# Kernel optimization log

Measured on AMD Instinct MI355X. Metric: run time of the kernel, lower is better.

The kernel has to match this reference:

```python
import jax, jax.numpy as jnp
import numpy as np

B, S, D, H, F, L, V, SPAN = 4, 1024, 1024, 16, 4096, 4, 32000, 512
DH = D // H
NEG = -1e9


def _ln(x, g, b, eps=1e-12):
    m = x.mean(-1, keepdims=True)
    v = ((x - m) ** 2).mean(-1, keepdims=True)
    return (x - m) * jax.lax.rsqrt(v + eps) * g + b


def setup_inputs() -> dict:
    key = jax.random.key(0)
    ks = iter(jax.random.split(key, 40))
    g = lambda shape: jax.random.normal(next(ks), shape, jnp.float32) * 0.02
    inp = {
        "input_ids": jax.random.randint(next(ks), (B, S), 0, V),
        "segment_ids": jnp.zeros((B, S), jnp.int32),
        "attention_mask": jnp.ones((B, S), jnp.float32),
        "tok_emb": g((V, D)),
        "seg_emb": g((2, D)),
        "emb_ln_g": jnp.ones((D,), jnp.float32),
        "emb_ln_b": jnp.zeros((D,), jnp.float32),
        "rel_emb": g((2 * SPAN, D)),
        "Wq": g((L, D, D)), "bq": jnp.zeros((L, D), jnp.float32),
        "Wk": g((L, D, D)), "bk": jnp.zeros((L, D), jnp.float32),
        "Wv": g((L, D, D)), "bv": jnp.zeros((L, D), jnp.float32),
        "Wo": g((L, D, D)), "bo": jnp.zeros((L, D), jnp.float32),
        "ln1_g": jnp.ones((L, D), jnp.float32), "ln1_b": jnp.zeros((L, D), jnp.float32),
        "W1": g((L, D, F)), "b1": jnp.zeros((L, F), jnp.float32),
        "W2": g((L, F, D)), "b2": jnp.zeros((L, D), jnp.float32),
        "ln2_g": jnp.ones((L, D), jnp.float32), "ln2_b": jnp.zeros((L, D), jnp.float32),
    }
    return inp


def _forward(input_ids, segment_ids, attention_mask, tok_emb, seg_emb, emb_ln_g,
             emb_ln_b, rel_emb, Wq, bq, Wk, bk, Wv, bv, Wo, bo, ln1_g, ln1_b,
             W1, b1, W2, b2, ln2_g, ln2_b):
    # BertEmbedding (max_len=0 => no absolute positions): token + segment, LN, mask
    h = _ln(tok_emb[input_ids] + seg_emb[segment_ids], emb_ln_g, emb_ln_b)
    h = h * attention_mask[..., None]

    # relative positions (bucket_size=0 path): rel[q,k] = q - k, clamped into table
    pos = jnp.arange(S)
    rel = pos[:, None] - pos[None, :]                      # [S,S]
    c2p_idx = jnp.clip(rel + SPAN, 0, 2 * SPAN - 1)        # [S,S]
    p2c_idx = jnp.clip(-rel + SPAN, 0, 2 * SPAN - 1)       # [S,S]
    bias = (1.0 - attention_mask)[:, None, None, :] * NEG  # [B,1,1,S] additive mask

    scale = 1.0 / jnp.sqrt(jnp.asarray(DH * 3, h.dtype))   # scale_factor = 1 + |{c2p,p2c}|

    def layer(h, p):
        wq, bq_, wk, bk_, wv, bv_, wo, bo_, g1, b1n, w1, b1f, w2, b2f, g2, b2n = p
        q = (h @ wq + bq_).reshape(B, S, H, DH)
        k = (h @ wk + bk_).reshape(B, S, H, DH)
        v = (h @ wv + bv_).reshape(B, S, H, DH)
        att = jnp.einsum('bqhd,bkhd->bhqk', q, k) * scale
        # disentangled relative-position bias (shared q/k projections on rel table)
        pos_k = (rel_emb @ wk + bk_).reshape(2 * SPAN, H, DH)
        pos_q = (rel_emb @ wq + bq_).reshape(2 * SPAN, H, DH)
        c2p = jnp.einsum('bqhd,phd->bhqp', q, pos_k) * scale   # [B,H,S,2*SPAN]
        att = att + jnp.take_along_axis(c2p, c2p_idx[None, None], axis=-1)
        p2c = jnp.einsum('bkhd,phd->bhkp', k, pos_q) * scale   # [B,H,S,2*SPAN]
        att = att + jnp.swapaxes(
            jnp.take_along_axis(p2c, p2c_idx[None, None], axis=-1), -1, -2)
        probs = jax.nn.softmax(att + bias, axis=-1)
        ctx = jnp.einsum('bhqk,bkhd->bqhd', probs, v).reshape(B, S, D)
        h = _ln(h + ctx @ wo + bo_, g1, b1n)
        ff = jax.nn.gelu(h @ w1 + b1f, approximate=False) @ w2 + b2f
        return _ln(h + ff, g2, b2n), None

    h, _ = jax.lax.scan(layer, h, (Wq, bq, Wk, bk, Wv, bv, Wo, bo,
                                   ln1_g, ln1_b, W1, b1, W2, b2, ln2_g, ln2_b))
    return h


def reference(input_ids, segment_ids, attention_mask, tok_emb, seg_emb, emb_ln_g,
              emb_ln_b, rel_emb, Wq, bq, Wk, bk, Wv, bv, Wo, bo, ln1_g, ln1_b,
              W1, b1, W2, b2, ln2_g, ln2_b):
    return _forward(input_ids, segment_ids, attention_mask, tok_emb, seg_emb,
                    emb_ln_g, emb_ln_b, rel_emb, Wq, bq, Wk, bk, Wv, bv, Wo, bo,
                    ln1_g, ln1_b, W1, b1, W2, b2, ln2_g, ln2_b)
```

## Files before the change

kernel.cpp:

```cpp
#include <hip/hip_runtime.h>

#define DEV __device__ __forceinline__

typedef __bf16 bf16;
typedef __bf16 bf16x4 __attribute__((ext_vector_type(4)));
typedef __bf16 bf16x8 __attribute__((ext_vector_type(8)));
typedef float f32x4 __attribute__((ext_vector_type(4)));

constexpr int B_ = 4, S_ = 1024, D_ = 1024, H_ = 16, F_ = 4096, L_ = 4, SPAN_ = 512, DH_ = 64;
constexpr float SCALE_ = 0.07216878364870322f;
constexpr float LOG2E_ = 1.4426950408889634f;
constexpr float SCL2_ = SCALE_ * LOG2E_;
constexpr float THR2_ = 11.5f;
constexpr long POSL_ = 32L * 1024 * 64;

DEV void gload_lds16(const void* g, void* l) {
  __builtin_amdgcn_global_load_lds((const __attribute__((address_space(1))) void*)g,
                                   (__attribute__((address_space(3))) void*)l, 16, 0, 0);
}

template <int CTRL>
DEV float dppf(float x) {
  return __builtin_bit_cast(
      float, __builtin_amdgcn_mov_dpp(__builtin_bit_cast(int, x), CTRL, 0xf, 0xf, true));
}
DEV float rowMax16(float v) {
  v = fmaxf(v, dppf<0x128>(v));
  v = fmaxf(v, dppf<0x124>(v));
  v = fmaxf(v, dppf<0x122>(v));
  v = fmaxf(v, dppf<0x121>(v));
  return v;
}
DEV float rowSum16(float v) {
  v += dppf<0x128>(v);
  v += dppf<0x124>(v);
  v += dppf<0x122>(v);
  v += dppf<0x121>(v);
  return v;
}

DEV float blockSum4(float v, volatile float* red) {
#pragma unroll
  for (int o = 32; o; o >>= 1) v += __shfl_xor(v, o);
  if ((threadIdx.x & 63) == 0) red[threadIdx.x >> 6] = v;
  __syncthreads();
  return red[0] + red[1] + red[2] + red[3];
}

DEV bf16x8 lds_frag(const bf16* buf, int row, int chunk) {
  return *(const bf16x8*)((const char*)buf + row * 128 + ((chunk ^ (row & 7)) << 4));
}
DEV bf16x8 rdfrag(const char* base, int row, int chunk) {
  return *(const bf16x8*)(base + row * 128 + ((chunk ^ (row & 7)) << 4));
}

template <int EPI>
__global__ __launch_bounds__(512, 1) void gemm256(
    const bf16* __restrict__ A, const bf16* __restrict__ Bm,
    const float* __restrict__ bias, void* __restrict__ Cout,
    int K, int lda, int ldb, int ldc, long sA, long sB, long sC) {
  extern __shared__ __align__(16) char smem[];

  const int z = blockIdx.z;
  A += (long)z * sA;
  Bm += (long)z * sB;
  const long coff = (long)z * sC;

  const int nwg = gridDim.x * gridDim.y;
  const int flat = blockIdx.y * gridDim.x + blockIdx.x;
  const int qq = nwg >> 3;
  const int swz = (flat & 7) * qq + (flat >> 3);
  const int bx = swz % gridDim.x, by = swz / gridDim.x;
  const int m0 = by * 256, n0 = bx * 256;

  const int tid = threadIdx.x, lane = tid & 63, wave = tid >> 6;
  const int wr = wave >> 2, wc = wave & 3;
  const int fr = lane & 15, fq = lane >> 4;

  f32x4 acc[8][4];
#pragma unroll
  for (int m = 0; m < 8; m++)
#pragma unroll
    for (int n = 0; n < 4; n++) acc[m][n] = f32x4{0.f, 0.f, 0.f, 0.f};

  const int r8 = tid >> 3;
  const int swzel = ((tid & 7) ^ (r8 & 7)) << 3;
  const bf16* ga = A + (long)(m0 + r8) * lda + swzel;
  const bf16* gb = Bm + (long)(n0 + r8) * ldb + swzel;

  const int NT = K >> 6;

  auto stage = [&](int t) {
    const long ko = (long)t * 64;
    char* da = smem + ((t & 1) << 15) + wave * 1024;
    gload_lds16(ga + ko, da);
    gload_lds16(ga + 64 * (long)lda + ko, da + 8192);
    gload_lds16(ga + 128 * (long)lda + ko, da + 16384);
    gload_lds16(ga + 192 * (long)lda + ko, da + 24576);
    char* db = smem + 65536 + ((t & 1) << 15) + wave * 1024;
    gload_lds16(gb + ko, db);
    gload_lds16(gb + 64 * (long)ldb + ko, db + 8192);
    gload_lds16(gb + 128 * (long)ldb + ko, db + 16384);
    gload_lds16(gb + 192 * (long)ldb + ko, db + 24576);
  };

  stage(0);
  asm volatile("s_waitcnt vmcnt(0)" ::: "memory");
  __builtin_amdgcn_s_barrier();

  for (int j = 0; j < NT; j++) {
    const char* Ac = smem + ((j & 1) << 15);
    const char* Bc = smem + 65536 + ((j & 1) << 15);

    if (j + 1 < NT) stage(j + 1);

    bf16x8 af[4][2], bfg[4][2];
#pragma unroll
    for (int m = 0; m < 4; m++) {
      const int ar = wr * 128 + m * 16 + fr;
      af[m][0] = rdfrag(Ac, ar, fq);
      af[m][1] = rdfrag(Ac, ar, 4 + fq);
    }
#pragma unroll
    for (int n = 0; n < 4; n++) {
      const int br = wc * 64 + n * 16 + fr;
      bfg[n][0] = rdfrag(Bc, br, fq);
      bfg[n][1] = rdfrag(Bc, br, 4 + fq);
    }

    __builtin_amdgcn_s_setprio(1);
#pragma unroll
    for (int m = 0; m < 4; m++)
#pragma unroll
      for (int n = 0; n < 4; n++)
#pragma unroll
        for (int kc = 0; kc < 2; kc++)
          acc[m][n] = __builtin_amdgcn_mfma_f32_16x16x32_bf16(af[m][kc], bfg[n][kc],
                                                              acc[m][n], 0, 0, 0);
    __builtin_amdgcn_s_setprio(0);
    __builtin_amdgcn_sched_barrier(0);

#pragma unroll
    for (int m = 0; m < 4; m++) {
      const int ar = wr * 128 + (m + 4) * 16 + fr;
      af[m][0] = rdfrag(Ac, ar, fq);
      af[m][1] = rdfrag(Ac, ar, 4 + fq);
    }
    __builtin_amdgcn_s_setprio(1);
#pragma unroll
    for (int m = 0; m < 4; m++)
#pragma unroll
      for (int n = 0; n < 4; n++)
#pragma unroll
        for (int kc = 0; kc < 2; kc++)
          acc[m + 4][n] = __builtin_amdgcn_mfma_f32_16x16x32_bf16(af[m][kc], bfg[n][kc],
                                                                  acc[m + 4][n], 0, 0, 0);
    __builtin_amdgcn_s_setprio(0);

    asm volatile("s_waitcnt vmcnt(0)" ::: "memory");
    __builtin_amdgcn_s_barrier();
  }

#pragma unroll
  for (int m = 0; m < 8; m++) {
#pragma unroll
    for (int n = 0; n < 4; n++) {
      const int col = n0 + wc * 64 + n * 16 + fr;
      float bval = 0.f;
      if constexpr (EPI == 3 || EPI == 4) bval = bias ? bias[col] : 0.f;
#pragma unroll
      for (int rr = 0; rr < 4; rr++) {
        const int row = m0 + wr * 128 + m * 16 + fq * 4 + rr;
        const long idx = coff + (long)row * ldc + col;
        const float v = acc[m][n][rr];
        if constexpr (EPI == 0) ((float*)Cout)[idx] = v;
        else if constexpr (EPI == 3) ((bf16*)Cout)[idx] = (bf16)(v + bval);
        else if constexpr (EPI == 4) {
          float x = v + bval;
          x = 0.5f * x * (1.f + erff(x * 0.70710678118654752f));
          ((bf16*)Cout)[idx] = (bf16)x;
        }
      }
    }
  }
}

template <int EPI>
__global__ __launch_bounds__(256) void gemm_bt(
    const bf16* __restrict__ A, const bf16* __restrict__ Bm,
    const float* __restrict__ bias, void* __restrict__ Cout,
    int M, int N, int K, int lda, int ldb, int ldc, float alpha,
    long sA, long sB, long sC, long sBias) {
  __shared__ alignas(16) bf16 As[128 * 64];
  __shared__ alignas(16) bf16 Bs[128 * 64];

  const int z = blockIdx.z;
  A += (long)z * sA;
  Bm += (long)z * sB;
  bias += (long)z * sBias;
  const long coff = (long)z * sC;

  const int nwg = gridDim.x * gridDim.y;
  const int flat = blockIdx.y * gridDim.x + blockIdx.x;
  const int qq = nwg >> 3;
  const int swz = (flat & 7) * qq + (flat >> 3);
  const int bx = swz % gridDim.x, by = swz / gridDim.x;

  const int m0 = by * 128, n0 = bx * 128;
  const int tid = threadIdx.x, lane = tid & 63, wave = tid >> 6;
  const int wr = wave >> 1, wc = wave & 1;
  const int fr = lane & 15, fq = lane >> 4;

  f32x4 acc[4][4];
#pragma unroll
  for (int m = 0; m < 4; m++)
#pragma unroll
    for (int n = 0; n < 4; n++) acc[m][n] = f32x4{0.f, 0.f, 0.f, 0.f};

  const int r8 = tid >> 3;
  const int swzel = ((tid & 7) ^ (r8 & 7)) << 3;
  const bf16* ga = A + (long)(m0 + r8) * lda + swzel;
  const bf16* gb = Bm + (long)(n0 + r8) * ldb + swzel;
  const int swzrd = fr & 7;

  for (int k0 = 0; k0 < K; k0 += 64) {
#pragma unroll
    for (int i = 0; i < 4; i++)
      gload_lds16(ga + (long)i * 32 * lda + k0, (char*)As + i * 4096 + wave * 1024);
#pragma unroll
    for (int i = 0; i < 4; i++)
      gload_lds16(gb + (long)i * 32 * ldb + k0, (char*)Bs + i * 4096 + wave * 1024);
    __syncthreads();
#pragma unroll
    for (int kc = 0; kc < 2; kc++) {
      bf16x8 af[4], bfv[4];
#pragma unroll
      for (int m = 0; m < 4; m++)
        af[m] = *(const bf16x8*)((char*)As + (wr * 64 + m * 16 + fr) * 128 +
                                 (((kc * 4 + fq) ^ swzrd) << 4));
#pragma unroll
      for (int n = 0; n < 4; n++)
        bfv[n] = *(const bf16x8*)((char*)Bs + (wc * 64 + n * 16 + fr) * 128 +
                                  (((kc * 4 + fq) ^ swzrd) << 4));
#pragma unroll
      for (int m = 0; m < 4; m++)
#pragma unroll
        for (int n = 0; n < 4; n++)
          acc[m][n] = __builtin_amdgcn_mfma_f32_16x16x32_bf16(af[m], bfv[n], acc[m][n], 0, 0, 0);
    }
    __syncthreads();
  }

#pragma unroll
  for (int m = 0; m < 4; m++) {
#pragma unroll
    for (int n = 0; n < 4; n++) {
      const int col = n0 + wc * 64 + n * 16 + fr;
      float bval = 0.f;
      if constexpr (EPI == 3 || EPI == 4 || EPI == 5) bval = bias ? bias[col] : 0.f;
#pragma unroll
      for (int rr = 0; rr < 4; rr++) {
        const int row = m0 + wr * 64 + m * 16 + fq * 4 + rr;
        const long idx = coff + (long)row * ldc + col;
        const float v = acc[m][n][rr];
        if constexpr (EPI == 0) ((float*)Cout)[idx] = v * alpha;
        else if constexpr (EPI == 3) ((bf16*)Cout)[idx] = (bf16)(v + bval);
        else if constexpr (EPI == 4) {
          float x = v + bval;
          x = 0.5f * x * (1.f + erff(x * 0.70710678118654752f));
          ((bf16*)Cout)[idx] = (bf16)x;
        } else if constexpr (EPI == 5) {
          const long pidx = coff + ((long)(col >> 6) * 1024 + row) * 64 + (col & 63);
          ((bf16*)Cout)[pidx] = (bf16)(v + bval);
        }
      }
    }
  }
}

__global__ __launch_bounds__(256) void repack_kv(const bf16* __restrict__ qkv,
                                                 bf16* __restrict__ kp,
                                                 bf16* __restrict__ vp) {
  const int kt = blockIdx.x, bh = blockIdx.y;
  const int b = bh >> 4, h = bh & 15;
  const int k0 = kt * 64;
  __shared__ bf16 t[64][72];
  const int ty = threadIdx.x >> 3, tx = threadIdx.x & 7;
#pragma unroll
  for (int p = 0; p < 2; p++) {
    const int s = k0 + p * 32 + ty;
    const long base = (long)(b * 1024 + s) * 3072 + h * 64;
    bf16x8 kv = *(const bf16x8*)(qkv + base + 1024 + tx * 8);
    *(bf16x8*)(kp + ((long)(bh * 1024 + s) << 6) + tx * 8) = kv;
    bf16x8 vv = *(const bf16x8*)(qkv + base + 2048 + tx * 8);
    *(bf16x8*)(&t[p * 32 + ty][tx * 8]) = vv;
  }
  __syncthreads();
  const int dh = threadIdx.x >> 2, sc = (threadIdx.x & 3) * 16;
  bf16 tmp[16];
#pragma unroll
  for (int j = 0; j < 16; j++) tmp[j] = t[sc + j][dh];
  bf16* dst = vp + ((long)(bh * 16 + kt) << 12) + dh * 64 + sc;
  *(bf16x8*)dst = *(bf16x8*)tmp;
  *(bf16x8*)(dst + 8) = *(bf16x8*)(tmp + 8);
}

__global__ __launch_bounds__(256) void attn_fused(
    const bf16* __restrict__ qkv, const bf16* __restrict__ kp,
    const bf16* __restrict__ vp, const bf16* __restrict__ pospk,
    const float* __restrict__ mask, bf16* __restrict__ ctx) {
  const int id = blockIdx.x;
  const int xcd = id & 7, sub = id >> 3;
  const int bh = xcd + 8 * (sub >> 4);
  const int qt = sub & 15;
  const int b = bh >> 4, h = bh & 15;
  const int q0 = qt * 64;
  const int tid = threadIdx.x, wave = tid >> 6, lane = tid & 63;
  const int fr = lane & 15, fq = lane >> 4;

  __shared__ alignas(16) char smem[79360];
  bf16* PXk = (bf16*)smem;
  char* p_l = smem;
  bf16* PXq = (bf16*)(smem + 16384);
  bf16* Ks = (bf16*)(smem + 32768);
  bf16* Vs = (bf16*)(smem + 40960);
  bf16* c2p_T = (bf16*)(smem + 49152);
  bf16* p2c_T = (bf16*)(smem + 61952);

  const bf16* posq = pospk + ((long)h << 16);
  const bf16* posk = pospk + ((long)(16 + h) << 16);
  const bf16* kbase = kp + ((long)bh << 16);
  const bf16* vbase = vp + ((long)bh << 16);

  bf16x8 qa[2];
  {
    const bf16* qrow = qkv + (long)(b * 1024 + q0 + wave * 16 + fr) * 3072 + h * 64;
    qa[0] = *(const bf16x8*)(qrow + fq * 8);
    qa[1] = *(const bf16x8*)(qrow + 32 + fq * 8);
  }

  f32x4 o[4];
#pragma unroll
  for (int n = 0; n < 4; n++) o[n] = f32x4{0.f, 0.f, 0.f, 0.f};
  float m_r[4], l_r[4];
#pragma unroll
  for (int r = 0; r < 4; r++) { m_r[r] = -1e30f; l_r[r] = 0.f; }

  char* pl_base = p_l + wave * 2048;
  bf16* c2p_w = c2p_T + wave * 1600;
  const int wbyte = wave * 1024;

  for (int kt = 0; kt < 16; kt++) {
    const int k0 = kt * 64;

    __syncthreads();
    {
      const int j0k = q0 - k0 + 449;
      const int j0q = k0 - q0 + 449;
#pragma unroll
      for (int c = 0; c < 4; c++) {
        const int u = c * 256 + tid;
        const int rr = u >> 3;
        const int sel = (((u & 7) ^ (rr & 7)) << 3);
        int jk = j0k + rr;
        jk = jk < 0 ? 0 : (jk > 1023 ? 1023 : jk);
        gload_lds16(posk + ((long)jk << 6) + sel, (char*)PXk + c * 4096 + wbyte);
        int jq = j0q + rr;
        jq = jq < 0 ? 0 : (jq > 1023 ? 1023 : jq);
        gload_lds16(posq + ((long)jq << 6) + sel, (char*)PXq + c * 4096 + wbyte);
      }
#pragma unroll
      for (int c = 0; c < 2; c++) {
        const int u = c * 256 + tid;
        const int rr = u >> 3;
        const int sel = (((u & 7) ^ (rr & 7)) << 3);
        gload_lds16(kbase + ((long)(k0 + rr) << 6) + sel, (char*)Ks + c * 4096 + wbyte);
        gload_lds16(vbase + ((long)kt << 12) + ((long)rr << 6) + sel,
                    (char*)Vs + c * 4096 + wbyte);
      }
    }
    __syncthreads();

    bf16x8 ka[2];
    ka[0] = lds_frag(Ks, wave * 16 + fr, fq);
    ka[1] = lds_frag(Ks, wave * 16 + fr, 4 + fq);
    __builtin_amdgcn_s_setprio(1);
    {
      f32x4 cw[5];
#pragma unroll
      for (int t = 0; t < 5; t++) cw[t] = f32x4{0.f, 0.f, 0.f, 0.f};
#pragma unroll
      for (int kc = 0; kc < 2; kc++)
#pragma unroll
        for (int t = 0; t < 5; t++) {
          const bf16x8 pb = lds_frag(PXk, wave * 16 + t * 16 + fr, kc * 4 + fq);
          cw[t] = __builtin_amdgcn_mfma_f32_16x16x32_bf16(qa[kc], pb, cw[t], 0, 0, 0);
        }
#pragma unroll
      for (int t = 0; t < 5; t++) {
        bf16x4 pk;
#pragma unroll
        for (int r = 0; r < 4; r++) pk[r] = (bf16)cw[t][r];
        *(bf16x4*)&c2p_w[(t * 16 + fr) * 20 + fq * 4] = pk;
      }
    }
    f32x4 s[4];
#pragma unroll
    for (int n = 0; n < 4; n++) s[n] = f32x4{0.f, 0.f, 0.f, 0.f};
#pragma unroll
    for (int kc = 0; kc < 2; kc++)
#pragma unroll
      for (int n = 0; n < 4; n++) {
        const bf16x8 kb = lds_frag(Ks, n * 16 + fr, kc * 4 + fq);
        s[n] = __builtin_amdgcn_mfma_f32_16x16x32_bf16(qa[kc], kb, s[n], 0, 0, 0);
      }
    {
      f32x4 pw[5];
#pragma unroll
      for (int t = 0; t < 5; t++) pw[t] = f32x4{0.f, 0.f, 0.f, 0.f};
#pragma unroll
      for (int kc = 0; kc < 2; kc++)
#pragma unroll
        for (int t = 0; t < 5; t++) {
          const bf16x8 pb = lds_frag(PXq, (wave + t) * 16 + fr, kc * 4 + fq);
          pw[t] = __builtin_amdgcn_mfma_f32_16x16x32_bf16(ka[kc], pb, pw[t], 0, 0, 0);
        }
#pragma unroll
      for (int t = 0; t < 5; t++) {
        bf16x4 pk;
#pragma unroll
        for (int r = 0; r < 4; r++) pk[r] = (bf16)pw[t][r];
        *(bf16x4*)&p2c_T[((wave + t) * 16 + fr) * 68 + wave * 16 + fq * 4] = pk;
      }
    }
    __builtin_amdgcn_s_setprio(0);
    __syncthreads();

    bf16x8 vb[2][4];
#pragma unroll
    for (int kc = 0; kc < 2; kc++)
#pragma unroll
      for (int n = 0; n < 4; n++) vb[kc][n] = lds_frag(Vs, n * 16 + fr, kc * 4 + fq);

    float st[4][4];
#pragma unroll
    for (int n = 0; n < 4; n++) {
      const int ki = n * 16 + fr;
      const float mb = (1.0f - mask[b * S_ + k0 + ki]) * (-1e9f * LOG2E_);
#pragma unroll
      for (int r = 0; r < 4; r++) {
        const int qi_s = fq * 4 + r;
        const float cv = (float)c2p_w[(qi_s - ki + 63) * 20 + qi_s];
        const float pv = (float)p2c_T[(ki - (wave * 16 + qi_s) + 63) * 68 + ki];
        st[n][r] = (s[n][r] + cv + pv) * SCL2_ + mb;
      }
    }

    float pmax[4];
#pragma unroll
    for (int r = 0; r < 4; r++) {
      float v = fmaxf(fmaxf(st[0][r], st[1][r]), fmaxf(st[2][r], st[3][r]));
      pmax[r] = rowMax16(v);
    }
    const bool ok = (pmax[0] - m_r[0] <= THR2_) && (pmax[1] - m_r[1] <= THR2_) &&
                    (pmax[2] - m_r[2] <= THR2_) && (pmax[3] - m_r[3] <= THR2_);
    if (!__all(ok)) {
#pragma unroll
      for (int r = 0; r < 4; r++) {
        const float mn = fmaxf(m_r[r], pmax[r]);
        const float sc = exp2f(m_r[r] - mn);
        m_r[r] = mn;
        l_r[r] *= sc;
#pragma unroll
        for (int n = 0; n < 4; n++) o[n][r] *= sc;
      }
    }
    float rs[4] = {0.f, 0.f, 0.f, 0.f};
#pragma unroll
    for (int n = 0; n < 4; n++) {
      const int ki = n * 16 + fr;
#pragma unroll
      for (int r = 0; r < 4; r++) {
        const int qi_s = fq * 4 + r;
        const float p = exp2f(st[n][r] - m_r[r]);
        rs[r] += p;
        *(bf16*)(pl_base + qi_s * 128 + ((ki * 2) ^ ((qi_s & 7) << 4))) = (bf16)p;
      }
    }
#pragma unroll
    for (int r = 0; r < 4; r++) l_r[r] += rowSum16(rs[r]);

#pragma unroll
    for (int kc = 0; kc < 2; kc++) {
      const bf16x8 pa =
          *(const bf16x8*)(pl_base + fr * 128 + ((kc * 64 + fq * 16) ^ ((fr & 7) << 4)));
#pragma unroll
      for (int n = 0; n < 4; n++)
        o[n] = __builtin_amdgcn_mfma_f32_16x16x32_bf16(pa, vb[kc][n], o[n], 0, 0, 0);
    }
  }

#pragma unroll
  for (int r = 0; r < 4; r++) {
    const float inv = 1.f / l_r[r];
    const long row = (long)(b * S_ + q0 + wave * 16 + fq * 4 + r) * D_ + h * 64;
#pragma unroll
    for (int n = 0; n < 4; n++) ctx[row + n * 16 + fr] = (bf16)(o[n][r] * inv);
  }
}

__global__ __launch_bounds__(256) void wtrans(const float* __restrict__ W,
                                              bf16* __restrict__ WT, int K, int N,
                                              long sW, long sT) {
  W += (long)blockIdx.z * sW;
  WT += (long)blockIdx.z * sT;
  __shared__ float t[32][33];
  const int n0 = blockIdx.x * 32, k0 = blockIdx.y * 32;
  const int tx = threadIdx.x & 31, ty = threadIdx.x >> 5;
#pragma unroll
  for (int i = ty; i < 32; i += 8) t[i][tx] = W[(long)(k0 + i) * N + n0 + tx];
  __syncthreads();
#pragma unroll
  for (int i = ty; i < 32; i += 8) WT[(long)(n0 + i) * K + k0 + tx] = (bf16)t[tx][i];
}

__global__ __launch_bounds__(256) void f2b(const float* __restrict__ in,
                                           bf16* __restrict__ out, long n) {
  long i = (long)blockIdx.x * 256 + threadIdx.x;
  if (i < n) out[i] = (bf16)in[i];
}

__global__ __launch_bounds__(256) void bias_concat(const float* __restrict__ bq,
                                                   const float* __restrict__ bk,
                                                   const float* __restrict__ bv,
                                                   float* __restrict__ bqkv) {
  const int i = blockIdx.x * 256 + threadIdx.x;
  const int l = i / (3 * D_), s = (i % (3 * D_)) / D_, d = i % D_;
  const float* src = s == 0 ? bq : (s == 1 ? bk : bv);
  bqkv[i] = src[l * D_ + d];
}

__global__ __launch_bounds__(256) void embed_ln(
    const int* __restrict__ ids, const int* __restrict__ segs,
    const float* __restrict__ mask, const float* __restrict__ tok,
    const float* __restrict__ seg, const float* __restrict__ g,
    const float* __restrict__ bta, float* __restrict__ h, bf16* __restrict__ hb) {
  __shared__ float r1[4], r2[4];
  const int t = blockIdx.x;
  const int d4 = threadIdx.x;
  const long tb4 = (long)ids[t] * 256;
  const long sb4 = (long)segs[t] * 256;
  const long b4 = (long)t * 256;
  f32x4 x = ((const f32x4*)tok)[tb4 + d4];
  const f32x4 sv = ((const f32x4*)seg)[sb4 + d4];
#pragma unroll
  for (int r = 0; r < 4; r++) x[r] += sv[r];
  float sm = x[0] + x[1] + x[2] + x[3];
  sm = blockSum4(sm, r1);
  const float mean = sm * (1.f / D_);
  float vs = 0.f;
#pragma unroll
  for (int r = 0; r < 4; r++) {
    const float c = x[r] - mean;
    vs += c * c;
  }
  vs = blockSum4(vs, r2);
  const float rstd = rsqrtf(vs * (1.f / D_) + 1e-12f);
  const float mk = mask[t];
  const f32x4 gv = ((const f32x4*)g)[d4];
  const f32x4 bv = ((const f32x4*)bta)[d4];
  f32x4 y;
  bf16x4 yb;
#pragma unroll
  for (int r = 0; r < 4; r++) {
    y[r] = ((x[r] - mean) * rstd * gv[r] + bv[r]) * mk;
    yb[r] = (bf16)y[r];
  }
  ((f32x4*)h)[b4 + d4] = y;
  *(bf16x4*)&hb[(b4 + d4) * 4] = yb;
}

template <int P>
__global__ __launch_bounds__(256) void ln_residual_red(
    const float* __restrict__ hin, float* __restrict__ hout,
    const float* __restrict__ part, long pstride4,
    const float* __restrict__ bias, const float* __restrict__ g,
    const float* __restrict__ bta, bf16* __restrict__ hb) {
  __shared__ float r1[4], r2[4];
  const int d4 = threadIdx.x;
  const long b4 = (long)blockIdx.x * 256;
  f32x4 x = ((const f32x4*)hin)[b4 + d4];
  const f32x4 bi = ((const f32x4*)bias)[d4];
#pragma unroll
  for (int r = 0; r < 4; r++) x[r] += bi[r];
#pragma unroll
  for (int z = 0; z < P; z++) {
    const f32x4 pv = ((const f32x4*)part)[(long)z * pstride4 + b4 + d4];
#pragma unroll
    for (int r = 0; r < 4; r++) x[r] += pv[r];
  }
  float sm = x[0] + x[1] + x[2] + x[3];
  sm = blockSum4(sm, r1);
  const float mean = sm * (1.f / D_);
  float vs = 0.f;
#pragma unroll
  for (int r = 0; r < 4; r++) {
    const float c = x[r] - mean;
    vs += c * c;
  }
  vs = blockSum4(vs, r2);
  const float rstd = rsqrtf(vs * (1.f / D_) + 1e-12f);
  const f32x4 gv = ((const f32x4*)g)[d4];
  const f32x4 bv = ((const f32x4*)bta)[d4];
  f32x4 y;
  bf16x4 yb;
#pragma unroll
  for (int r = 0; r < 4; r++) {
    y[r] = (x[r] - mean) * rstd * gv[r] + bv[r];
    yb[r] = (bf16)y[r];
  }
  ((f32x4*)hout)[b4 + d4] = y;
  *(bf16x4*)&hb[(b4 + d4) * 4] = yb;
}

extern "C" void kernel_launch(void* const* d_in, const int* in_sizes, int n_in,
                              void* d_out, int out_size, void* d_ws, size_t ws_size,
                              hipStream_t stream) {
  (void)in_sizes; (void)n_in; (void)out_size; (void)ws_size;
  const int* input_ids = (const int*)d_in[0];
  const int* segment_ids = (const int*)d_in[1];
  const float* attention_mask = (const float*)d_in[2];
  const float* tok_emb = (const float*)d_in[3];
  const float* seg_emb = (const float*)d_in[4];
  const float* emb_ln_g = (const float*)d_in[5];
  const float* emb_ln_b = (const float*)d_in[6];
  const float* rel_emb = (const float*)d_in[7];
  const float* Wq = (const float*)d_in[8];
  const float* bq = (const float*)d_in[9];
  const float* Wk = (const float*)d_in[10];
  const float* bk = (const float*)d_in[11];
  const float* Wv = (const float*)d_in[12];
  const float* bv = (const float*)d_in[13];
  const float* Wo = (const float*)d_in[14];
  const float* bo = (const float*)d_in[15];
  const float* ln1_g = (const float*)d_in[16];
  const float* ln1_b = (const float*)d_in[17];
  const float* W1 = (const float*)d_in[18];
  const float* b1 = (const float*)d_in[19];
  const float* W2 = (const float*)d_in[20];
  const float* b2 = (const float*)d_in[21];
  const float* ln2_g = (const float*)d_in[22];
  const float* ln2_b = (const float*)d_in[23];

  const long DD = (long)D_ * D_;
  const long DF = (long)D_ * F_;
  const int D3 = 3 * D_;

  char* ws = (char*)d_ws;
  auto alloc = [&](size_t bytes) {
    char* p = ws;
    ws += (bytes + 255) & ~(size_t)255;
    return p;
  };
  bf16* wqkvT = (bf16*)alloc((size_t)L_ * 3 * DD * 2);
  bf16* woT = (bf16*)alloc((size_t)L_ * DD * 2);
  bf16* w1T = (bf16*)alloc((size_t)L_ * DF * 2);
  bf16* w2T = (bf16*)alloc((size_t)L_ * DF * 2);
  float* bqkv = (float*)alloc((size_t)L_ * 3 * D_ * 4);
  bf16* relb = (bf16*)alloc((size_t)2 * SPAN_ * D_ * 2);
  float* hbuf = (float*)alloc((size_t)B_ * S_ * D_ * 4);
  bf16* hb = (bf16*)alloc((size_t)B_ * S_ * D_ * 2);
  bf16* qkv = (bf16*)alloc((size_t)B_ * S_ * 3 * D_ * 2);
  bf16* kp = (bf16*)alloc((size_t)B_ * H_ * S_ * DH_ * 2);
  bf16* vp = (bf16*)alloc((size_t)B_ * H_ * S_ * DH_ * 2);
  bf16* pospk = (bf16*)alloc((size_t)L_ * POSL_ * 2);
  bf16* ctxb = (bf16*)alloc((size_t)B_ * S_ * D_ * 2);
  bf16* ff1b = (bf16*)alloc((size_t)B_ * S_ * F_ * 2);
  float* kpart = (float*)alloc((size_t)4 * B_ * S_ * D_ * 4);
  const long PSTR = (long)B_ * S_ * D_;

  wtrans<<<dim3(D_ / 32, D_ / 32, L_), 256, 0, stream>>>(Wq, wqkvT + 0 * DD, D_, D_, DD, 3 * DD);
  wtrans<<<dim3(D_ / 32, D_ / 32, L_), 256, 0, stream>>>(Wk, wqkvT + 1 * DD, D_, D_, DD, 3 * DD);
  wtrans<<<dim3(D_ / 32, D_ / 32, L_), 256, 0, stream>>>(Wv, wqkvT + 2 * DD, D_, D_, DD, 3 * DD);
  wtrans<<<dim3(D_ / 32, D_ / 32, L_), 256, 0, stream>>>(Wo, woT, D_, D_, DD, DD);
  wtrans<<<dim3(F_ / 32, D_ / 32, L_), 256, 0, stream>>>(W1, w1T, D_, F_, DF, DF);
  wtrans<<<dim3(D_ / 32, F_ / 32, L_), 256, 0, stream>>>(W2, w2T, F_, D_, DF, DF);
  bias_concat<<<dim3(L_ * 3 * D_ / 256), 256, 0, stream>>>(bq, bk, bv, bqkv);
  f2b<<<dim3((2 * SPAN_ * D_) / 256), 256, 0, stream>>>(rel_emb, relb, (long)2 * SPAN_ * D_);
  gemm_bt<5><<<dim3((2 * D_) / 128, (2 * SPAN_) / 128, L_), 256, 0, stream>>>(
      relb, wqkvT, bqkv, pospk, 2 * SPAN_, 2 * D_, D_, D_, D_, 0, 1.f,
      0, 3 * DD, POSL_, 3 * D_);
  embed_ln<<<dim3(B_ * S_), 256, 0, stream>>>(input_ids, segment_ids, attention_mask,
                                              tok_emb, seg_emb, emb_ln_g, emb_ln_b, hbuf, hb);

  const size_t SH = 131072;

  for (int l = 0; l < L_; ++l) {
    const bf16* wqkv_ = wqkvT + (long)l * 3 * DD;
    const bf16* wo_ = woT + (long)l * DD;
    const bf16* w1_ = w1T + (long)l * DF;
    const bf16* w2_ = w2T + (long)l * DF;
    const float* bqkv_ = bqkv + (long)l * 3 * D_;
    const float* bo_ = bo + (long)l * D_;
    const float* b1_ = b1 + (long)l * F_;
    const float* b2_ = b2 + (long)l * D_;

    gemm256<3><<<dim3(D3 / 256, (B_ * S_) / 256, 1), 512, SH, stream>>>(
        hb, wqkv_, bqkv_, qkv, D_, D_, D_, D3, 0, 0, 0);
    repack_kv<<<dim3(16, B_ * H_), 256, 0, stream>>>(qkv, kp, vp);

    attn_fused<<<dim3(1024), 256, 0, stream>>>(qkv, kp, vp, pospk + (long)l * POSL_,
                                               attention_mask, ctxb);

    gemm_bt<0><<<dim3(D_ / 128, (B_ * S_) / 128, 1), 256, 0, stream>>>(
        ctxb, wo_, nullptr, kpart, B_ * S_, D_, D_, D_, D_, D_, 1.f, 0, 0, 0, 0);
    ln_residual_red<1><<<dim3(B_ * S_), 256, 0, stream>>>(
        hbuf, hbuf, kpart, 0, bo_, ln1_g + l * D_, ln1_b + l * D_, hb);

    gemm256<4><<<dim3(F_ / 256, (B_ * S_) / 256, 1), 512, SH, stream>>>(
        hb, w1_, b1_, ff1b, D_, D_, D_, F_, 0, 0, 0);
    gemm256<0><<<dim3(D_ / 256, (B_ * S_) / 256, 4), 512, SH, stream>>>(
        ff1b, w2_, nullptr, kpart, F_ / 4, F_, F_, D_, F_ / 4, F_ / 4, PSTR);
    float* hout = (l == L_ - 1) ? (float*)d_out : hbuf;
    ln_residual_red<4><<<dim3(B_ * S_), 256, 0, stream>>>(
        hbuf, hout, kpart, PSTR / 4, b2_, ln2_g + l * D_, ln2_b + l * D_, hb);
  }
}
```

Before: 1.334 ms.

## Split attention tile staging into two async phases overlapping loads with MFMA work

Splits the per-tile global-to-LDS staging into two groups: PXk and K for the next tile are prefetched right after the p2c phase, while PXq and V for the current tile are issued at loop start and only awaited before the p2c MFMAs via partial vmcnt waits and raw barriers. The P scratch buffer moves to overlap the PXq region so the early prefetch into PXk does not collide with it. The mask loads are hoisted ahead of the waits. This is meant to hide load latency behind the c2p and QK computation, at the cost of more barriers and tricky vmcnt accounting that could race if the counts are wrong.

```diff
diff --git a/kernel.cpp b/kernel.cpp
--- a/kernel.cpp
+++ b/kernel.cpp
@@ -320,8 +320,8 @@
 
   __shared__ alignas(16) char smem[79360];
   bf16* PXk = (bf16*)smem;
-  char* p_l = smem;
   bf16* PXq = (bf16*)(smem + 16384);
+  char* p_l = smem + 16384;
   bf16* Ks = (bf16*)(smem + 32768);
   bf16* Vs = (bf16*)(smem + 40960);
   bf16* c2p_T = (bf16*)(smem + 49152);
@@ -350,36 +350,59 @@
   bf16* c2p_w = c2p_T + wave * 1600;
   const int wbyte = wave * 1024;
 
+  auto stage_pxk_ks = [&](int t) {
+    const int kk0 = t * 64;
+    const int j0k = q0 - kk0 + 449;
+#pragma unroll
+    for (int c = 0; c < 4; c++) {
+      const int u = c * 256 + tid;
+      const int rr = u >> 3;
+      const int sel = (((u & 7) ^ (rr & 7)) << 3);
+      int jk = j0k + rr;
+      jk = jk < 0 ? 0 : (jk > 1023 ? 1023 : jk);
+      gload_lds16(posk + ((long)jk << 6) + sel, (char*)PXk + c * 4096 + wbyte);
+    }
+#pragma unroll
+    for (int c = 0; c < 2; c++) {
+      const int u = c * 256 + tid;
+      const int rr = u >> 3;
+      const int sel = (((u & 7) ^ (rr & 7)) << 3);
+      gload_lds16(kbase + ((long)(kk0 + rr) << 6) + sel, (char*)Ks + c * 4096 + wbyte);
+    }
+  };
+  auto stage_pxq_vs = [&](int t) {
+    const int kk0 = t * 64;
+    const int j0q = kk0 - q0 + 449;
+#pragma unroll
+    for (int c = 0; c < 4; c++) {
+      const int u = c * 256 + tid;
+      const int rr = u >> 3;
+      const int sel = (((u & 7) ^ (rr & 7)) << 3);
+      int jq = j0q + rr;
+      jq = jq < 0 ? 0 : (jq > 1023 ? 1023 : jq);
+      gload_lds16(posq + ((long)jq << 6) + sel, (char*)PXq + c * 4096 + wbyte);
+    }
+#pragma unroll
+    for (int c = 0; c < 2; c++) {
+      const int u = c * 256 + tid;
+      const int rr = u >> 3;
+      const int sel = (((u & 7) ^ (rr & 7)) << 3);
+      gload_lds16(vbase + ((long)t << 12) + ((long)rr << 6) + sel,
+                  (char*)Vs + c * 4096 + wbyte);
+    }
+  };
+
+  stage_pxk_ks(0);
+
   for (int kt = 0; kt < 16; kt++) {
     const int k0 = kt * 64;
 
-    __syncthreads();
-    {
-      const int j0k = q0 - k0 + 449;
-      const int j0q = k0 - q0 + 449;
-#pragma unroll
-      for (int c = 0; c < 4; c++) {
-        const int u = c * 256 + tid;
-        const int rr = u >> 3;
-        const int sel = (((u & 7) ^ (rr & 7)) << 3);
-        int jk = j0k + rr;
-        jk = jk < 0 ? 0 : (jk > 1023 ? 1023 : jk);
-        gload_lds16(posk + ((long)jk << 6) + sel, (char*)PXk + c * 4096 + wbyte);
-        int jq = j0q + rr;
-        jq = jq < 0 ? 0 : (jq > 1023 ? 1023 : jq);
-        gload_lds16(posq + ((long)jq << 6) + sel, (char*)PXq + c * 4096 + wbyte);
-      }
-#pragma unroll
-      for (int c = 0; c < 2; c++) {
-        const int u = c * 256 + tid;
-        const int rr = u >> 3;
-        const int sel = (((u & 7) ^ (rr & 7)) << 3);
-        gload_lds16(kbase + ((long)(k0 + rr) << 6) + sel, (char*)Ks + c * 4096 + wbyte);
-        gload_lds16(vbase + ((long)kt << 12) + ((long)rr << 6) + sel,
-                    (char*)Vs + c * 4096 + wbyte);
-      }
-    }
-    __syncthreads();
+    float mraw[4];
+#pragma unroll
+    for (int n = 0; n < 4; n++) mraw[n] = mask[b * S_ + k0 + n * 16 + fr];
+    stage_pxq_vs(kt);
+    asm volatile("s_waitcnt vmcnt(10)" ::: "memory");
+    __builtin_amdgcn_s_barrier();
 
     bf16x8 ka[2];
     ka[0] = lds_frag(Ks, wave * 16 + fr, fq);
@@ -414,6 +437,12 @@
         const bf16x8 kb = lds_frag(Ks, n * 16 + fr, kc * 4 + fq);
         s[n] = __builtin_amdgcn_mfma_f32_16x16x32_bf16(qa[kc], kb, s[n], 0, 0, 0);
       }
+    __builtin_amdgcn_s_setprio(0);
+
+    asm volatile("s_waitcnt vmcnt(0)" ::: "memory");
+    __builtin_amdgcn_s_barrier();
+
+    __builtin_amdgcn_s_setprio(1);
     {
       f32x4 pw[5];
 #pragma unroll
@@ -436,6 +465,8 @@
     __builtin_amdgcn_s_setprio(0);
     __syncthreads();
 
+    if (kt < 15) stage_pxk_ks(kt + 1);
+
     bf16x8 vb[2][4];
 #pragma unroll
     for (int kc = 0; kc < 2; kc++)
@@ -445,11 +476,11 @@
     float st[4][4];
 #pragma unroll
     for (int n = 0; n < 4; n++) {
-      const int ki = n * 16 + fr;
-      const float mb = (1.0f - mask[b * S_ + k0 + ki]) * (-1e9f * LOG2E_);
+      const float mb = (1.0f - mraw[n]) * (-1e9f * LOG2E_);
 #pragma unroll
       for (int r = 0; r < 4; r++) {
         const int qi_s = fq * 4 + r;
+        const int ki = n * 16 + fr;
         const float cv = (float)c2p_w[(qi_s - ki + 63) * 20 + qi_s];
         const float pv = (float)p2c_T[(ki - (wave * 16 + qi_s) + 63) * 68 + ki];
         st[n][r] = (s[n][r] + cv + pv) * SCL2_ + mb;
@@ -498,6 +529,8 @@
       for (int n = 0; n < 4; n++)
         o[n] = __builtin_amdgcn_mfma_f32_16x16x32_bf16(pa, vb[kc][n], o[n], 0, 0, 0);
     }
+
+    __builtin_amdgcn_s_barrier();
   }
 
 #pragma unroll
```

Measured after the change: 1.355 ms. No clear change (+1.5%).
